# Kernel optimization log

Hardware: AMD Instinct MI355X
Metric: run time of the kernel (lower is better)

## Reference

```python
import jax, jax.numpy as jnp
import numpy as np

B, D_IN, D_CTX, UNITS, RANK = 4096, 2048, 512, 2048, 256


def setup_inputs() -> dict:
    key = jax.random.key(0)
    ks = jax.random.split(key, 6)
    scale_u = 1.0 / np.sqrt(D_IN)
    scale_w = 1.0 / np.sqrt(D_CTX)
    return {
        "inputs": jax.random.normal(ks[0], (B, D_IN), dtype=jnp.float32),
        "context": jax.random.normal(ks[1], (B, D_CTX), dtype=jnp.float32),
        "U": jax.random.normal(ks[2], (D_IN, RANK), dtype=jnp.float32) * scale_u,
        "S": jax.random.uniform(ks[3], (RANK,), dtype=jnp.float32) + 0.5,
        "V": jax.random.normal(ks[4], (UNITS, RANK), dtype=jnp.float32) * scale_u,
        "W": jax.random.normal(ks[5], (D_CTX, RANK), dtype=jnp.float32) * scale_w,
        "Bc": jnp.zeros((RANK,), dtype=jnp.float32),
        "bias": jnp.zeros((UNITS,), dtype=jnp.float32),
    }


def reference(inputs, context, U, S, V, W, Bc, bias):
    # h = context @ W + Bc ; chi = sigmoid(h) ; s[b,r] = S[r] * chi[b,r]
    chi = jax.nn.sigmoid(context @ W + Bc)           # [B, R]
    s = S * chi                                       # [B, R]
    # Original math: out[b,m] = sum_{n,r} x[b,n] U[n,r] s[b,r] V[m,r]
    # Reassociated (identical math, no [B,N,M] kernel): ((x @ U) * s) @ V^T
    proj = (inputs @ U) * s                           # [B, R]
    out = proj @ V.T + bias                           # [B, UNITS]
    return out  # activation is linear (None)
```

## Files before the change

kernel.cpp:

```cpp
#include <hip/hip_runtime.h>
#include <math.h>

namespace {

constexpr int Bdim  = 4096;
constexpr int D_IN  = 2048;
constexpr int D_CTX = 512;
constexpr int UNITS = 2048;
constexpr int RANK  = 256;
constexpr int SPLIT = 8;

typedef __bf16 bf16x8 __attribute__((ext_vector_type(8)));
typedef float  f32x4  __attribute__((ext_vector_type(4)));

__global__ __launch_bounds__(256) void k_prep(
    const float* __restrict__ U, const float* __restrict__ W,
    __bf16* __restrict__ Ut, __bf16* __restrict__ Wt) {
  const int job = blockIdx.y;
  const int t = threadIdx.x;
  const float* src = job ? W : U;
  __bf16* dst      = job ? Wt : Ut;
  const int K = job ? D_CTX : D_IN;
  const int tilesK = K / 64;
  const int tid = blockIdx.x;
  if (tid >= tilesK * 4) return;
  const int k0 = (tid % tilesK) * 64;
  const int n0 = (tid / tilesK) * 64;
  __shared__ __bf16 T[64][72];
  const int i  = t >> 4;
  const int j4 = (t & 15) * 4;
  for (int ii = i; ii < 64; ii += 16) {
    float4 v = *(const float4*)(src + (size_t)(k0 + ii) * RANK + n0 + j4);
    T[j4 + 0][ii] = (__bf16)v.x;
    T[j4 + 1][ii] = (__bf16)v.y;
    T[j4 + 2][ii] = (__bf16)v.z;
    T[j4 + 3][ii] = (__bf16)v.w;
  }
  __syncthreads();
  const int jj = t >> 3;
  const int c  = t & 7;
  for (int j2 = jj; j2 < 64; j2 += 32) {
    bf16x8 v = *(const bf16x8*)&T[j2][c * 8];
    *(bf16x8*)(dst + (size_t)(n0 + j2) * K + k0 + c * 8) = v;
  }
}

__global__ __launch_bounds__(256) void k_pg(
    const float* __restrict__ x,   const __bf16* __restrict__ Ut,
    const float* __restrict__ ctx, const __bf16* __restrict__ Wt,
    const float* __restrict__ S,   const float* __restrict__ Bc,
    __bf16* __restrict__ part, __bf16* __restrict__ s_out) {
  constexpr int BM = 32, BN = 256, BK = 64;
  __shared__ __align__(16) __bf16 As[BM * BK];
  __shared__ __align__(16) __bf16 Bs[BN * BK];
  const int t = threadIdx.x;
  const bool gate = (blockIdx.y == 0);
  const int slice = (int)blockIdx.y - 1;
  const int bm = blockIdx.x * BM;
  const float*  A = gate ? ctx : x;
  const __bf16* B = gate ? Wt  : Ut;
  const int Kt   = gate ? D_CTX : D_IN;
  const int k_lo = gate ? 0 : slice * (D_IN / SPLIT);
  const int k_hi = gate ? D_CTX : k_lo + (D_IN / SPLIT);
  const int w = t >> 6, l = t & 63;
  const int wc0 = w * 64;
  const int lrow = l & 15;
  const int lk   = l >> 4;
  f32x4 acc[2][4] = {};

  float4 a_lo, a_hi;
  bf16x8 b_bf[8];
  const int srow = t >> 3, skc = t & 7;

  auto LOADA = [&](int k0) {
    const float* g = A + (size_t)(bm + srow) * Kt + k0 + skc * 8;
    a_lo = *(const float4*)g;
    a_hi = *(const float4*)(g + 4);
  };
  auto LOADB = [&](int k0) {
#pragma unroll
    for (int ci = 0; ci < 8; ++ci) {
      const int c = t + ci * 256;
      const int row = c >> 3, kc = c & 7;
      b_bf[ci] = *(const bf16x8*)(B + (size_t)row * Kt + k0 + kc * 8);
    }
  };
  auto WRITEA = [&]() {
    bf16x8 v;
    v[0] = (__bf16)a_lo.x; v[1] = (__bf16)a_lo.y;
    v[2] = (__bf16)a_lo.z; v[3] = (__bf16)a_lo.w;
    v[4] = (__bf16)a_hi.x; v[5] = (__bf16)a_hi.y;
    v[6] = (__bf16)a_hi.z; v[7] = (__bf16)a_hi.w;
    *(bf16x8*)((char*)As + srow * 128 + ((skc ^ (srow & 7)) * 16)) = v;
  };
  auto WRITEB = [&]() {
#pragma unroll
    for (int ci = 0; ci < 8; ++ci) {
      const int c = t + ci * 256;
      const int row = c >> 3, kc = c & 7;
      *(bf16x8*)((char*)Bs + row * 128 + ((kc ^ (row & 7)) * 16)) = b_bf[ci];
    }
  };

  LOADA(k_lo);
  LOADB(k_lo);
  for (int k0 = k_lo; k0 < k_hi; k0 += BK) {
    WRITEA();
    WRITEB();
    __syncthreads();
    if (k0 + BK < k_hi) {
      LOADA(k0 + BK);
      LOADB(k0 + BK);
    }
#pragma unroll
    for (int kk = 0; kk < 2; ++kk) {
      bf16x8 af[2], bfr[4];
#pragma unroll
      for (int mf = 0; mf < 2; ++mf) {
        const int row = mf * 16 + lrow;
        af[mf] = *(const bf16x8*)((const char*)As + row * 128 +
                                  (((kk * 4 + lk) ^ (row & 7)) * 16));
      }
#pragma unroll
      for (int nf = 0; nf < 4; ++nf) {
        const int row = wc0 + nf * 16 + lrow;
        bfr[nf] = *(const bf16x8*)((const char*)Bs + row * 128 +
                                   (((kk * 4 + lk) ^ (row & 7)) * 16));
      }
#pragma unroll
      for (int mf = 0; mf < 2; ++mf)
#pragma unroll
        for (int nf = 0; nf < 4; ++nf)
          acc[mf][nf] = __builtin_amdgcn_mfma_f32_16x16x32_bf16(
              af[mf], bfr[nf], acc[mf][nf], 0, 0, 0);
    }
    __syncthreads();
  }

#pragma unroll
  for (int mf = 0; mf < 2; ++mf) {
#pragma unroll
    for (int nf = 0; nf < 4; ++nf) {
#pragma unroll
      for (int r = 0; r < 4; ++r) {
        const int m = bm + mf * 16 + lk * 4 + r;
        const int n = wc0 + nf * 16 + lrow;
        const float val = acc[mf][nf][r];
        if (gate) {
          const float h = val + Bc[n];
          s_out[(size_t)m * RANK + n] = (__bf16)(S[n] / (1.0f + __expf(-h)));
        } else {
          part[((size_t)slice * Bdim + m) * RANK + n] = (__bf16)val;
        }
      }
    }
  }
}

__global__ __launch_bounds__(256) void k_combine(
    const __bf16* __restrict__ part, const __bf16* __restrict__ s,
    __bf16* __restrict__ proj) {
  const size_t i8 = ((size_t)blockIdx.x * 256 + threadIdx.x) * 8;
  float sum[8] = {};
#pragma unroll
  for (int sl = 0; sl < SPLIT; ++sl) {
    bf16x8 v = *(const bf16x8*)(part + (size_t)sl * Bdim * RANK + i8);
#pragma unroll
    for (int i = 0; i < 8; ++i) sum[i] += (float)v[i];
  }
  bf16x8 sv = *(const bf16x8*)(s + i8);
  bf16x8 o;
#pragma unroll
  for (int i = 0; i < 8; ++i) o[i] = (__bf16)(sum[i] * (float)sv[i]);
  *(bf16x8*)(proj + i8) = o;
}

__global__ __launch_bounds__(256) void k_out(
    const __bf16* __restrict__ proj, const float* __restrict__ V,
    const float* __restrict__ bias, float* __restrict__ out) {
  constexpr int BM = 128, BN = 128, BK = 64;
  constexpr int Kt = RANK;
  __shared__ __align__(16) __bf16 As[BM * BK];
  __shared__ __align__(16) __bf16 Bs[BN * BK];
  const int t = threadIdx.x;
  const int lin = (int)(blockIdx.y * gridDim.x + blockIdx.x);
  const int swz = (lin & 7) * 64 + (lin >> 3);
  const int bm = (swz & 31) * BM;
  const int bn = (swz >> 5) * BN;
  const int w = t >> 6, l = t & 63;
  const int wr0 = (w >> 1) * 64;
  const int wc0 = (w & 1) * 64;
  const int lrow = l & 15;
  const int lk   = l >> 4;
  f32x4 acc[4][4] = {};

  bf16x8 a_bf[4];
  float4 b_lo[4], b_hi[4];

  auto LOADA = [&](int k0) {
#pragma unroll
    for (int ci = 0; ci < 4; ++ci) {
      const int c = t + ci * 256;
      const int row = c >> 3, kc = c & 7;
      a_bf[ci] = *(const bf16x8*)(proj + (size_t)(bm + row) * Kt + k0 + kc * 8);
    }
  };
  auto LOADB = [&](int k0) {
#pragma unroll
    for (int ci = 0; ci < 4; ++ci) {
      const int c = t + ci * 256;
      const int row = c >> 3, kc = c & 7;
      const float* g = V + (size_t)(bn + row) * Kt + k0 + kc * 8;
      b_lo[ci] = *(const float4*)g;
      b_hi[ci] = *(const float4*)(g + 4);
    }
  };
  auto WRITEA = [&]() {
#pragma unroll
    for (int ci = 0; ci < 4; ++ci) {
      const int c = t + ci * 256;
      const int row = c >> 3, kc = c & 7;
      *(bf16x8*)((char*)As + row * 128 + ((kc ^ (row & 7)) * 16)) = a_bf[ci];
    }
  };
  auto WRITEB = [&]() {
#pragma unroll
    for (int ci = 0; ci < 4; ++ci) {
      const int c = t + ci * 256;
      const int row = c >> 3, kc = c & 7;
      bf16x8 v;
      v[0] = (__bf16)b_lo[ci].x; v[1] = (__bf16)b_lo[ci].y;
      v[2] = (__bf16)b_lo[ci].z; v[3] = (__bf16)b_lo[ci].w;
      v[4] = (__bf16)b_hi[ci].x; v[5] = (__bf16)b_hi[ci].y;
      v[6] = (__bf16)b_hi[ci].z; v[7] = (__bf16)b_hi[ci].w;
      *(bf16x8*)((char*)Bs + row * 128 + ((kc ^ (row & 7)) * 16)) = v;
    }
  };

  LOADA(0);
  LOADB(0);
  for (int k0 = 0; k0 < Kt; k0 += BK) {
    WRITEA();
    WRITEB();
    __syncthreads();
    if (k0 + BK < Kt) {
      LOADA(k0 + BK);
      LOADB(k0 + BK);
    }
#pragma unroll
    for (int kk = 0; kk < 2; ++kk) {
      bf16x8 af[4], bfr[4];
#pragma unroll
      for (int mf = 0; mf < 4; ++mf) {
        const int row = wr0 + mf * 16 + lrow;
        af[mf] = *(const bf16x8*)((const char*)As + row * 128 +
                                  (((kk * 4 + lk) ^ (row & 7)) * 16));
      }
#pragma unroll
      for (int nf = 0; nf < 4; ++nf) {
        const int row = wc0 + nf * 16 + lrow;
        bfr[nf] = *(const bf16x8*)((const char*)Bs + row * 128 +
                                   (((kk * 4 + lk) ^ (row & 7)) * 16));
      }
#pragma unroll
      for (int mf = 0; mf < 4; ++mf)
#pragma unroll
        for (int nf = 0; nf < 4; ++nf)
          acc[mf][nf] = __builtin_amdgcn_mfma_f32_16x16x32_bf16(
              af[mf], bfr[nf], acc[mf][nf], 0, 0, 0);
    }
    __syncthreads();
  }

#pragma unroll
  for (int mf = 0; mf < 4; ++mf) {
#pragma unroll
    for (int nf = 0; nf < 4; ++nf) {
#pragma unroll
      for (int r = 0; r < 4; ++r) {
        const int m = bm + wr0 + mf * 16 + lk * 4 + r;
        const int n = bn + wc0 + nf * 16 + lrow;
        out[(size_t)m * UNITS + n] = acc[mf][nf][r] + bias[n];
      }
    }
  }
}

}

extern "C" void kernel_launch(void* const* d_in, const int* in_sizes, int n_in,
                              void* d_out, int out_size, void* d_ws, size_t ws_size,
                              hipStream_t stream) {
  const float* inputs  = (const float*)d_in[0];
  const float* context = (const float*)d_in[1];
  const float* U       = (const float*)d_in[2];
  const float* S       = (const float*)d_in[3];
  const float* V       = (const float*)d_in[4];
  const float* W       = (const float*)d_in[5];
  const float* Bc      = (const float*)d_in[6];
  const float* bias    = (const float*)d_in[7];
  float* out = (float*)d_out;

  char* ws = (char*)d_ws;
  __bf16* Ut   = (__bf16*)(ws);
  __bf16* Wt   = (__bf16*)(ws + 1048576);
  __bf16* proj = (__bf16*)(ws + 1310720);
  __bf16* sbuf = (__bf16*)(ws + 3407872);
  __bf16* part = (__bf16*)(ws + 5505024);

  k_prep<<<dim3(128, 2), 256, 0, stream>>>(U, W, Ut, Wt);

  k_pg<<<dim3(Bdim / 32, SPLIT + 1), 256, 0, stream>>>(
      inputs, Ut, context, Wt, S, Bc, part, sbuf);

  k_combine<<<dim3((Bdim * RANK) / (256 * 8)), 256, 0, stream>>>(part, sbuf, proj);

  k_out<<<dim3(Bdim / 128, UNITS / 128), 256, 0, stream>>>(proj, V, bias, out);
}
```

Before: 49.00 us.

## Fuse split-K combine into output GEMM and halve k_pg N-tile

Removes the separate k_combine kernel: the output GEMM now sums the eight split-K partials, applies the gate scale, and writes the full 128x256 proj tile into shared memory before its K loop. k_pg is also retiled to BN=128 with a 2x2 warp layout, doubling its grid in y. This drops one launch and a proj round trip through global memory. The cost is that each of the 16 column blocks sharing a row block now re-reads and re-reduces the partials, adding redundant global traffic and a larger LDS footprint in k_out.

```diff
diff --git a/kernel.cpp b/kernel.cpp
--- a/kernel.cpp
+++ b/kernel.cpp
@@ -50,26 +50,30 @@
     const float* __restrict__ ctx, const __bf16* __restrict__ Wt,
     const float* __restrict__ S,   const float* __restrict__ Bc,
     __bf16* __restrict__ part, __bf16* __restrict__ s_out) {
-  constexpr int BM = 32, BN = 256, BK = 64;
+  constexpr int BM = 32, BN = 128, BK = 64;
   __shared__ __align__(16) __bf16 As[BM * BK];
   __shared__ __align__(16) __bf16 Bs[BN * BK];
   const int t = threadIdx.x;
-  const bool gate = (blockIdx.y == 0);
-  const int slice = (int)blockIdx.y - 1;
+  const int y = blockIdx.y;
+  const bool gate = (y < 2);
+  const int nh    = gate ? y : ((y - 2) & 1);
+  const int slice = (y - 2) >> 1;
   const int bm = blockIdx.x * BM;
+  const int bn = nh * BN;
   const float*  A = gate ? ctx : x;
   const __bf16* B = gate ? Wt  : Ut;
   const int Kt   = gate ? D_CTX : D_IN;
   const int k_lo = gate ? 0 : slice * (D_IN / SPLIT);
   const int k_hi = gate ? D_CTX : k_lo + (D_IN / SPLIT);
   const int w = t >> 6, l = t & 63;
-  const int wc0 = w * 64;
+  const int wr0 = (w >> 1) * 16;
+  const int wc0 = (w & 1) * 64;
   const int lrow = l & 15;
   const int lk   = l >> 4;
-  f32x4 acc[2][4] = {};
+  f32x4 acc[4] = {};
 
   float4 a_lo, a_hi;
-  bf16x8 b_bf[8];
+  bf16x8 b_bf[4];
   const int srow = t >> 3, skc = t & 7;
 
   auto LOADA = [&](int k0) {
@@ -79,10 +83,10 @@
   };
   auto LOADB = [&](int k0) {
 #pragma unroll
-    for (int ci = 0; ci < 8; ++ci) {
-      const int c = t + ci * 256;
-      const int row = c >> 3, kc = c & 7;
-      b_bf[ci] = *(const bf16x8*)(B + (size_t)row * Kt + k0 + kc * 8);
+    for (int ci = 0; ci < 4; ++ci) {
+      const int c = t + ci * 256;
+      const int row = c >> 3, kc = c & 7;
+      b_bf[ci] = *(const bf16x8*)(B + (size_t)(bn + row) * Kt + k0 + kc * 8);
     }
   };
   auto WRITEA = [&]() {
@@ -95,7 +99,7 @@
   };
   auto WRITEB = [&]() {
 #pragma unroll
-    for (int ci = 0; ci < 8; ++ci) {
+    for (int ci = 0; ci < 4; ++ci) {
       const int c = t + ci * 256;
       const int row = c >> 3, kc = c & 7;
       *(bf16x8*)((char*)Bs + row * 128 + ((kc ^ (row & 7)) * 16)) = b_bf[ci];
@@ -114,12 +118,11 @@
     }
 #pragma unroll
     for (int kk = 0; kk < 2; ++kk) {
-      bf16x8 af[2], bfr[4];
-#pragma unroll
-      for (int mf = 0; mf < 2; ++mf) {
-        const int row = mf * 16 + lrow;
-        af[mf] = *(const bf16x8*)((const char*)As + row * 128 +
-                                  (((kk * 4 + lk) ^ (row & 7)) * 16));
+      bf16x8 af, bfr[4];
+      {
+        const int row = wr0 + lrow;
+        af = *(const bf16x8*)((const char*)As + row * 128 +
+                              (((kk * 4 + lk) ^ (row & 7)) * 16));
       }
 #pragma unroll
       for (int nf = 0; nf < 4; ++nf) {
@@ -128,59 +131,36 @@
                                    (((kk * 4 + lk) ^ (row & 7)) * 16));
       }
 #pragma unroll
-      for (int mf = 0; mf < 2; ++mf)
-#pragma unroll
-        for (int nf = 0; nf < 4; ++nf)
-          acc[mf][nf] = __builtin_amdgcn_mfma_f32_16x16x32_bf16(
-              af[mf], bfr[nf], acc[mf][nf], 0, 0, 0);
-    }
-    __syncthreads();
-  }
-
-#pragma unroll
-  for (int mf = 0; mf < 2; ++mf) {
-#pragma unroll
-    for (int nf = 0; nf < 4; ++nf) {
-#pragma unroll
-      for (int r = 0; r < 4; ++r) {
-        const int m = bm + mf * 16 + lk * 4 + r;
-        const int n = wc0 + nf * 16 + lrow;
-        const float val = acc[mf][nf][r];
-        if (gate) {
-          const float h = val + Bc[n];
-          s_out[(size_t)m * RANK + n] = (__bf16)(S[n] / (1.0f + __expf(-h)));
-        } else {
-          part[((size_t)slice * Bdim + m) * RANK + n] = (__bf16)val;
-        }
-      }
-    }
-  }
-}
-
-__global__ __launch_bounds__(256) void k_combine(
+      for (int nf = 0; nf < 4; ++nf)
+        acc[nf] = __builtin_amdgcn_mfma_f32_16x16x32_bf16(af, bfr[nf], acc[nf], 0, 0, 0);
+    }
+    __syncthreads();
+  }
+
+#pragma unroll
+  for (int nf = 0; nf < 4; ++nf) {
+#pragma unroll
+    for (int r = 0; r < 4; ++r) {
+      const int m = bm + wr0 + lk * 4 + r;
+      const int n = bn + wc0 + nf * 16 + lrow;
+      const float val = acc[nf][r];
+      if (gate) {
+        const float h = val + Bc[n];
+        s_out[(size_t)m * RANK + n] = (__bf16)(S[n] / (1.0f + __expf(-h)));
+      } else {
+        part[((size_t)slice * Bdim + m) * RANK + n] = (__bf16)val;
+      }
+    }
+  }
+}
+
+__global__ __launch_bounds__(256) void k_out(
     const __bf16* __restrict__ part, const __bf16* __restrict__ s,
-    __bf16* __restrict__ proj) {
-  const size_t i8 = ((size_t)blockIdx.x * 256 + threadIdx.x) * 8;
-  float sum[8] = {};
-#pragma unroll
-  for (int sl = 0; sl < SPLIT; ++sl) {
-    bf16x8 v = *(const bf16x8*)(part + (size_t)sl * Bdim * RANK + i8);
-#pragma unroll
-    for (int i = 0; i < 8; ++i) sum[i] += (float)v[i];
-  }
-  bf16x8 sv = *(const bf16x8*)(s + i8);
-  bf16x8 o;
-#pragma unroll
-  for (int i = 0; i < 8; ++i) o[i] = (__bf16)(sum[i] * (float)sv[i]);
-  *(bf16x8*)(proj + i8) = o;
-}
-
-__global__ __launch_bounds__(256) void k_out(
-    const __bf16* __restrict__ proj, const float* __restrict__ V,
-    const float* __restrict__ bias, float* __restrict__ out) {
+    const float* __restrict__ V, const float* __restrict__ bias,
+    float* __restrict__ out) {
   constexpr int BM = 128, BN = 128, BK = 64;
   constexpr int Kt = RANK;
-  __shared__ __align__(16) __bf16 As[BM * BK];
+  __shared__ __align__(16) __bf16 As[BM * Kt];
   __shared__ __align__(16) __bf16 Bs[BN * BK];
   const int t = threadIdx.x;
   const int lin = (int)(blockIdx.y * gridDim.x + blockIdx.x);
@@ -194,17 +174,7 @@
   const int lk   = l >> 4;
   f32x4 acc[4][4] = {};
 
-  bf16x8 a_bf[4];
   float4 b_lo[4], b_hi[4];
-
-  auto LOADA = [&](int k0) {
-#pragma unroll
-    for (int ci = 0; ci < 4; ++ci) {
-      const int c = t + ci * 256;
-      const int row = c >> 3, kc = c & 7;
-      a_bf[ci] = *(const bf16x8*)(proj + (size_t)(bm + row) * Kt + k0 + kc * 8);
-    }
-  };
   auto LOADB = [&](int k0) {
 #pragma unroll
     for (int ci = 0; ci < 4; ++ci) {
@@ -213,14 +183,6 @@
       const float* g = V + (size_t)(bn + row) * Kt + k0 + kc * 8;
       b_lo[ci] = *(const float4*)g;
       b_hi[ci] = *(const float4*)(g + 4);
-    }
-  };
-  auto WRITEA = [&]() {
-#pragma unroll
-    for (int ci = 0; ci < 4; ++ci) {
-      const int c = t + ci * 256;
-      const int row = c >> 3, kc = c & 7;
-      *(bf16x8*)((char*)As + row * 128 + ((kc ^ (row & 7)) * 16)) = a_bf[ci];
     }
   };
   auto WRITEB = [&]() {
@@ -237,24 +199,39 @@
     }
   };
 
-  LOADA(0);
   LOADB(0);
+
+  for (int ci = 0; ci < 16; ++ci) {
+    const int c2  = t + ci * 256;
+    const int row = c2 >> 5;
+    const int kc  = c2 & 31;
+    float sum[8] = {};
+#pragma unroll
+    for (int sl = 0; sl < SPLIT; ++sl) {
+      bf16x8 v = *(const bf16x8*)(part + ((size_t)sl * Bdim + bm + row) * RANK + kc * 8);
+#pragma unroll
+      for (int i = 0; i < 8; ++i) sum[i] += (float)v[i];
+    }
+    bf16x8 sv = *(const bf16x8*)(s + (size_t)(bm + row) * RANK + kc * 8);
+    bf16x8 o;
+#pragma unroll
+    for (int i = 0; i < 8; ++i) o[i] = (__bf16)(sum[i] * (float)sv[i]);
+    *(bf16x8*)((char*)As + row * 512 + ((kc ^ (row & 7)) * 16)) = o;
+  }
+
   for (int k0 = 0; k0 < Kt; k0 += BK) {
-    WRITEA();
     WRITEB();
     __syncthreads();
-    if (k0 + BK < Kt) {
-      LOADA(k0 + BK);
-      LOADB(k0 + BK);
-    }
+    if (k0 + BK < Kt) LOADB(k0 + BK);
 #pragma unroll
     for (int kk = 0; kk < 2; ++kk) {
       bf16x8 af[4], bfr[4];
 #pragma unroll
       for (int mf = 0; mf < 4; ++mf) {
         const int row = wr0 + mf * 16 + lrow;
-        af[mf] = *(const bf16x8*)((const char*)As + row * 128 +
-                                  (((kk * 4 + lk) ^ (row & 7)) * 16));
+        const int cch = (k0 >> 3) + kk * 4 + lk;
+        af[mf] = *(const bf16x8*)((const char*)As + row * 512 +
+                                  ((cch ^ (row & 7)) * 16));
       }
 #pragma unroll
       for (int nf = 0; nf < 4; ++nf) {
@@ -304,16 +281,14 @@
   char* ws = (char*)d_ws;
   __bf16* Ut   = (__bf16*)(ws);
   __bf16* Wt   = (__bf16*)(ws + 1048576);
-  __bf16* proj = (__bf16*)(ws + 1310720);
-  __bf16* sbuf = (__bf16*)(ws + 3407872);
-  __bf16* part = (__bf16*)(ws + 5505024);
+  __bf16* sbuf = (__bf16*)(ws + 1310720);
+  __bf16* part = (__bf16*)(ws + 3407872);
 
   k_prep<<<dim3(128, 2), 256, 0, stream>>>(U, W, Ut, Wt);
 
-  k_pg<<<dim3(Bdim / 32, SPLIT + 1), 256, 0, stream>>>(
+  k_pg<<<dim3(Bdim / 32, 2 * SPLIT + 2), 256, 0, stream>>>(
       inputs, Ut, context, Wt, S, Bc, part, sbuf);
 
-  k_combine<<<dim3((Bdim * RANK) / (256 * 8)), 256, 0, stream>>>(part, sbuf, proj);
-
-  k_out<<<dim3(Bdim / 128, UNITS / 128), 256, 0, stream>>>(proj, V, bias, out);
-}
+  k_out<<<dim3(Bdim / 128, UNITS / 128), 256, 0, stream>>>(
+      part, sbuf, V, bias, out);
+}
```

Result: slower. 65.11 us (+32.9%).

## Split projection GEMM along N, halve K-split, double-buffer shared tiles

Applied to the files above, without the earlier changes.

The projection/gate GEMM kernel now tiles N into two 128-wide halves per block instead of one 256-wide tile, and halves the K split from 8 to 4 slices. The grid grows to 2*SPLIT+2 rows, and each warp now covers 16 rows by 64 columns. Shared-memory A/B tiles are double-buffered, which drops the trailing __syncthreads per K step. The aim is to cut partial-sum traffic in the combine kernel while keeping enough blocks for occupancy. It also cuts per-thread register use. The cost is that A tiles are re-read for each N half.

```diff
diff --git a/kernel.cpp b/kernel.cpp
--- a/kernel.cpp
+++ b/kernel.cpp
@@ -8,7 +8,7 @@
 constexpr int D_CTX = 512;
 constexpr int UNITS = 2048;
 constexpr int RANK  = 256;
-constexpr int SPLIT = 8;
+constexpr int SPLIT = 4;
 
 typedef __bf16 bf16x8 __attribute__((ext_vector_type(8)));
 typedef float  f32x4  __attribute__((ext_vector_type(4)));
@@ -50,26 +50,30 @@
     const float* __restrict__ ctx, const __bf16* __restrict__ Wt,
     const float* __restrict__ S,   const float* __restrict__ Bc,
     __bf16* __restrict__ part, __bf16* __restrict__ s_out) {
-  constexpr int BM = 32, BN = 256, BK = 64;
-  __shared__ __align__(16) __bf16 As[BM * BK];
-  __shared__ __align__(16) __bf16 Bs[BN * BK];
+  constexpr int BM = 32, BN = 128, BK = 64;
+  __shared__ __align__(16) __bf16 As[2][BM * BK];
+  __shared__ __align__(16) __bf16 Bs[2][BN * BK];
   const int t = threadIdx.x;
-  const bool gate = (blockIdx.y == 0);
-  const int slice = (int)blockIdx.y - 1;
+  const int y = blockIdx.y;
+  const bool gate = (y < 2);
+  const int nh    = gate ? y : ((y - 2) & 1);
+  const int slice = (y - 2) >> 1;
   const int bm = blockIdx.x * BM;
+  const int bn = nh * BN;
   const float*  A = gate ? ctx : x;
   const __bf16* B = gate ? Wt  : Ut;
   const int Kt   = gate ? D_CTX : D_IN;
   const int k_lo = gate ? 0 : slice * (D_IN / SPLIT);
   const int k_hi = gate ? D_CTX : k_lo + (D_IN / SPLIT);
   const int w = t >> 6, l = t & 63;
-  const int wc0 = w * 64;
+  const int wr0 = (w >> 1) * 16;
+  const int wc0 = (w & 1) * 64;
   const int lrow = l & 15;
   const int lk   = l >> 4;
-  f32x4 acc[2][4] = {};
+  f32x4 acc[4] = {};
 
   float4 a_lo, a_hi;
-  bf16x8 b_bf[8];
+  bf16x8 b_bf[4];
   const int srow = t >> 3, skc = t & 7;
 
   auto LOADA = [&](int k0) {
@@ -79,34 +83,35 @@
   };
   auto LOADB = [&](int k0) {
 #pragma unroll
-    for (int ci = 0; ci < 8; ++ci) {
-      const int c = t + ci * 256;
-      const int row = c >> 3, kc = c & 7;
-      b_bf[ci] = *(const bf16x8*)(B + (size_t)row * Kt + k0 + kc * 8);
-    }
-  };
-  auto WRITEA = [&]() {
+    for (int ci = 0; ci < 4; ++ci) {
+      const int c = t + ci * 256;
+      const int row = c >> 3, kc = c & 7;
+      b_bf[ci] = *(const bf16x8*)(B + (size_t)(bn + row) * Kt + k0 + kc * 8);
+    }
+  };
+  auto WRITEA = [&](int buf) {
     bf16x8 v;
     v[0] = (__bf16)a_lo.x; v[1] = (__bf16)a_lo.y;
     v[2] = (__bf16)a_lo.z; v[3] = (__bf16)a_lo.w;
     v[4] = (__bf16)a_hi.x; v[5] = (__bf16)a_hi.y;
     v[6] = (__bf16)a_hi.z; v[7] = (__bf16)a_hi.w;
-    *(bf16x8*)((char*)As + srow * 128 + ((skc ^ (srow & 7)) * 16)) = v;
-  };
-  auto WRITEB = [&]() {
-#pragma unroll
-    for (int ci = 0; ci < 8; ++ci) {
-      const int c = t + ci * 256;
-      const int row = c >> 3, kc = c & 7;
-      *(bf16x8*)((char*)Bs + row * 128 + ((kc ^ (row & 7)) * 16)) = b_bf[ci];
+    *(bf16x8*)((char*)As[buf] + srow * 128 + ((skc ^ (srow & 7)) * 16)) = v;
+  };
+  auto WRITEB = [&](int buf) {
+#pragma unroll
+    for (int ci = 0; ci < 4; ++ci) {
+      const int c = t + ci * 256;
+      const int row = c >> 3, kc = c & 7;
+      *(bf16x8*)((char*)Bs[buf] + row * 128 + ((kc ^ (row & 7)) * 16)) = b_bf[ci];
     }
   };
 
   LOADA(k_lo);
   LOADB(k_lo);
+  int cur = 0;
   for (int k0 = k_lo; k0 < k_hi; k0 += BK) {
-    WRITEA();
-    WRITEB();
+    WRITEA(cur);
+    WRITEB(cur);
     __syncthreads();
     if (k0 + BK < k_hi) {
       LOADA(k0 + BK);
@@ -114,44 +119,37 @@
     }
 #pragma unroll
     for (int kk = 0; kk < 2; ++kk) {
-      bf16x8 af[2], bfr[4];
-#pragma unroll
-      for (int mf = 0; mf < 2; ++mf) {
-        const int row = mf * 16 + lrow;
-        af[mf] = *(const bf16x8*)((const char*)As + row * 128 +
-                                  (((kk * 4 + lk) ^ (row & 7)) * 16));
+      bf16x8 af, bfr[4];
+      {
+        const int row = wr0 + lrow;
+        af = *(const bf16x8*)((const char*)As[cur] + row * 128 +
+                              (((kk * 4 + lk) ^ (row & 7)) * 16));
       }
 #pragma unroll
       for (int nf = 0; nf < 4; ++nf) {
         const int row = wc0 + nf * 16 + lrow;
-        bfr[nf] = *(const bf16x8*)((const char*)Bs + row * 128 +
+        bfr[nf] = *(const bf16x8*)((const char*)Bs[cur] + row * 128 +
                                    (((kk * 4 + lk) ^ (row & 7)) * 16));
       }
 #pragma unroll
-      for (int mf = 0; mf < 2; ++mf)
-#pragma unroll
-        for (int nf = 0; nf < 4; ++nf)
-          acc[mf][nf] = __builtin_amdgcn_mfma_f32_16x16x32_bf16(
-              af[mf], bfr[nf], acc[mf][nf], 0, 0, 0);
-    }
-    __syncthreads();
-  }
-
-#pragma unroll
-  for (int mf = 0; mf < 2; ++mf) {
-#pragma unroll
-    for (int nf = 0; nf < 4; ++nf) {
-#pragma unroll
-      for (int r = 0; r < 4; ++r) {
-        const int m = bm + mf * 16 + lk * 4 + r;
-        const int n = wc0 + nf * 16 + lrow;
-        const float val = acc[mf][nf][r];
-        if (gate) {
-          const float h = val + Bc[n];
-          s_out[(size_t)m * RANK + n] = (__bf16)(S[n] / (1.0f + __expf(-h)));
-        } else {
-          part[((size_t)slice * Bdim + m) * RANK + n] = (__bf16)val;
-        }
+      for (int nf = 0; nf < 4; ++nf)
+        acc[nf] = __builtin_amdgcn_mfma_f32_16x16x32_bf16(af, bfr[nf], acc[nf], 0, 0, 0);
+    }
+    cur ^= 1;
+  }
+
+#pragma unroll
+  for (int nf = 0; nf < 4; ++nf) {
+#pragma unroll
+    for (int r = 0; r < 4; ++r) {
+      const int m = bm + wr0 + lk * 4 + r;
+      const int n = bn + wc0 + nf * 16 + lrow;
+      const float val = acc[nf][r];
+      if (gate) {
+        const float h = val + Bc[n];
+        s_out[(size_t)m * RANK + n] = (__bf16)(S[n] / (1.0f + __expf(-h)));
+      } else {
+        part[((size_t)slice * Bdim + m) * RANK + n] = (__bf16)val;
       }
     }
   }
@@ -310,7 +308,7 @@
 
   k_prep<<<dim3(128, 2), 256, 0, stream>>>(U, W, Ut, Wt);
 
-  k_pg<<<dim3(Bdim / 32, SPLIT + 1), 256, 0, stream>>>(
+  k_pg<<<dim3(Bdim / 32, 2 * SPLIT + 2), 256, 0, stream>>>(
       inputs, Ut, context, Wt, S, Bc, part, sbuf);
 
   k_combine<<<dim3((Bdim * RANK) / (256 * 8)), 256, 0, stream>>>(part, sbuf, proj);
```

Result: faster. 47.30 us (-3.5%).
